# Optimization experiments

Measured on AMD Instinct MI355X. Metric: run time of the kernel, lower is better.

Reference implementation:

```python
import jax, jax.numpy as jnp
import numpy as np

EPS_STAB = 1e-9   # numerical_stabilizer default
BN_EPS = 1e-5     # flax BatchNorm default epsilon


def setup_inputs() -> dict:
    key = jax.random.key(0)
    ks = jax.random.split(key, 5)
    B, N, C = 2, 4096, 512
    s = 1.0 / np.sqrt(C)
    d = {"inputs": jax.random.normal(ks[0], (B, N, C), jnp.float32)}
    # 1x1 convs == pointwise linear maps [C_in, C_out] + bias
    for i, w in enumerate(["Wq", "Wk", "Wv", "Wo"]):
        d[w] = jax.random.normal(ks[1 + i], (C, C), jnp.float32) * s
    for b in ["bq", "bk", "bv", "bo"]:
        d[b] = jnp.zeros((C,), jnp.float32)
    # BatchNorm (inference: use_running_average=True since train=False)
    d["bn_scale"] = jnp.ones((C,), jnp.float32)
    d["bn_bias"] = jnp.zeros((C,), jnp.float32)
    d["bn_mean"] = jnp.zeros((C,), jnp.float32)
    d["bn_var"] = jnp.ones((C,), jnp.float32)
    return d


def reference(inputs, Wq, bq, Wk, bk, Wv, bv, Wo, bo,
              bn_scale, bn_bias, bn_mean, bn_var):
    # QKV via 1x1 conv == dense projection. [B, N, C]
    q = inputs @ Wq + bq
    k = inputs @ Wk + bk
    v = inputs @ Wv + bv
    # scores [B, M, N]; softmax over last axis (N)
    att = jax.nn.softmax(jnp.einsum('bmc,bnc->bmn', q, k), axis=-1)
    # non-standard renorm: divide by column sums (axis=1 == M axis)
    att = att / (EPS_STAB + jnp.sum(att, axis=1, keepdims=True))
    # faithful to einsum '...MN,...NC->...NC': sum attention over M, scale v
    out = v * jnp.sum(att, axis=1)[..., None]
    # output 1x1 conv
    out = out @ Wo + bo
    # BatchNorm with running stats (feature axis -1)
    out = (out - bn_mean) * jax.lax.rsqrt(bn_var + BN_EPS) * bn_scale + bn_bias
    return jax.nn.relu(out) + inputs
```

## Files before the change

### kernel.cpp

```cpp
#include <hip/hip_runtime.h>
#include <hip/hip_bf16.h>

typedef unsigned short u16;
typedef unsigned int u32;
typedef __attribute__((ext_vector_type(8))) short short8;
typedef __attribute__((ext_vector_type(4))) float f32x4;

__device__ __forceinline__ u16 f2bf(float f) {
    union { float f; unsigned u; } v; v.f = f;
    unsigned r = v.u + 0x7fffu + ((v.u >> 16) & 1u);
    return (u16)(r >> 16);
}

__device__ __forceinline__ float fexp2(float x) {
#if __has_builtin(__builtin_amdgcn_exp2f)
    return __builtin_amdgcn_exp2f(x);
#else
    return __expf(x * 0.6931471805599453f);
#endif
}

#if __has_builtin(__builtin_amdgcn_cvt_pk_fp8_f32) && \
    __has_builtin(__builtin_amdgcn_cvt_f32_fp8)
#define FP8_HW 1
#else
#define FP8_HW 0
#endif

#if !FP8_HW
__device__ __forceinline__ u32 sw_fp8(float x) {
    union { float f; u32 u; } v; v.f = x;
    int E = (int)(v.u >> 23) - 127;
    if (x < 0.001953125f) return 0;
    if (E < -6) return (u32)(x * 512.0f + 0.5f);
    u32 m = v.u & 0x7fffffu;
    u32 r = (m + 0x80000u) >> 20;
    u32 bits = ((u32)(E + 7) << 3) + r;
    return bits > 0x7eu ? 0x7eu : bits;
}
__device__ __forceinline__ float sw_fp8d(u32 b) {
    u32 e = (b >> 3) & 15u, m = b & 7u;
    if (e == 0) return (float)m * 0.001953125f;
    union { u32 u; float f; } v; v.u = ((e + 120u) << 23) | (m << 20);
    return v.f;
}
#endif

__device__ __forceinline__ u32 fp8x4_pack(float p0, float p1, float p2, float p3) {
#if FP8_HW
    u32 v = (u32)__builtin_amdgcn_cvt_pk_fp8_f32(p0, p1, 0, false);
    v = (u32)__builtin_amdgcn_cvt_pk_fp8_f32(p2, p3, (int)v, true);
    return v;
#else
    return sw_fp8(p0) | (sw_fp8(p1) << 8) | (sw_fp8(p2) << 16) | (sw_fp8(p3) << 24);
#endif
}

#if FP8_HW
#define FP8_DEC(v, s) __builtin_amdgcn_cvt_f32_fp8((int)(v), (s))
#else
#define FP8_DEC(v, s) sw_fp8d(((v) >> ((s) * 8)) & 0xffu)
#endif

__device__ __forceinline__ void async_cp16(const u16* g, u16* l) {
    __builtin_amdgcn_global_load_lds(
        (const __attribute__((address_space(1))) void*)g,
        (__attribute__((address_space(3))) void*)l, 16, 0, 0);
}


__device__ __forceinline__ void gemm512(const u16* __restrict__ A,
                                        const u16* __restrict__ B,
                                        u16* As, u16* Bs,
                                        f32x4 acc[4][4], int tid) {
    const int lane = tid & 63, w = tid >> 6;
    const int quad = lane >> 4, l15 = lane & 15;
    const int wm = tid >> 7, wn = (tid >> 6) & 1;
    const int Gw = lane ^ ((lane >> 3) & 7);
    const int srow = Gw >> 2;
    const int scol = (Gw & 3) * 8;
    const int arow0 = w * 32 + srow, arow1 = arow0 + 16;
    u16* la0 = As + (w * 2 + 0) * 512;
    u16* la1 = As + (w * 2 + 1) * 512;
    u16* lb0 = Bs + (w * 2 + 0) * 512;
    u16* lb1 = Bs + (w * 2 + 1) * 512;
    const int Pr8 = ((l15 * 4 + quad) ^ (l15 >> 1)) * 8;
    for (int k0 = 0; k0 < 512; k0 += 32) {
        __syncthreads();
        async_cp16(A + (size_t)arow0 * 512 + k0 + scol, la0);
        async_cp16(A + (size_t)arow1 * 512 + k0 + scol, la1);
        async_cp16(B + (size_t)arow0 * 512 + k0 + scol, lb0);
        async_cp16(B + (size_t)arow1 * 512 + k0 + scol, lb1);
        __syncthreads();
        short8 af[4], bfr[4];
#pragma unroll
        for (int i = 0; i < 4; i++)
            af[i] = *(const short8*)&As[(wm * 64 + i * 16) * 32 + Pr8];
#pragma unroll
        for (int j = 0; j < 4; j++)
            bfr[j] = *(const short8*)&Bs[(wn * 64 + j * 16) * 32 + Pr8];
#pragma unroll
        for (int i = 0; i < 4; i++)
#pragma unroll
            for (int j = 0; j < 4; j++)
                acc[i][j] = __builtin_amdgcn_mfma_f32_16x16x32_bf16(
                    af[i], bfr[j], acc[i][j], 0, 0, 0);
    }
}

__device__ __forceinline__ void gemm512_r64(const u16* __restrict__ A,
                                            const u16* __restrict__ B,
                                            u16* As, u16* Bs,
                                            f32x4 acc[2][4], int tid) {
    const int lane = tid & 63, w = tid >> 6;
    const int quad = lane >> 4, l15 = lane & 15;
    const int wm = tid >> 7, wn = (tid >> 6) & 1;
    const int Gw = lane ^ ((lane >> 3) & 7);
    const int srow = Gw >> 2;
    const int scol = (Gw & 3) * 8;
    const int arowA = w * 16 + srow;
    const int arowB0 = (w * 2 + 0) * 16 + srow;
    const int arowB1 = (w * 2 + 1) * 16 + srow;
    u16* la = As + w * 512;
    u16* lb0 = Bs + (w * 2 + 0) * 512;
    u16* lb1 = Bs + (w * 2 + 1) * 512;
    const int Pr8 = ((l15 * 4 + quad) ^ (l15 >> 1)) * 8;
    for (int k0 = 0; k0 < 512; k0 += 32) {
        __syncthreads();
        async_cp16(A + (size_t)arowA * 512 + k0 + scol, la);
        async_cp16(B + (size_t)arowB0 * 512 + k0 + scol, lb0);
        async_cp16(B + (size_t)arowB1 * 512 + k0 + scol, lb1);
        __syncthreads();
        short8 af[2], bfr[4];
#pragma unroll
        for (int i = 0; i < 2; i++)
            af[i] = *(const short8*)&As[(wm * 32 + i * 16) * 32 + Pr8];
#pragma unroll
        for (int j = 0; j < 4; j++)
            bfr[j] = *(const short8*)&Bs[(wn * 64 + j * 16) * 32 + Pr8];
#pragma unroll
        for (int i = 0; i < 2; i++)
#pragma unroll
            for (int j = 0; j < 4; j++)
                acc[i][j] = __builtin_amdgcn_mfma_f32_16x16x32_bf16(
                    af[i], bfr[j], acc[i][j], 0, 0, 0);
    }
}

__global__ void prep(const float* __restrict__ X, const float* __restrict__ W0,
                     const float* __restrict__ W1, const float* __restrict__ W2,
                     const float* __restrict__ W3, u16* __restrict__ Xb,
                     u16* __restrict__ T0, u16* __restrict__ T1,
                     u16* __restrict__ T2, u16* __restrict__ T3,
                     float* __restrict__ Sg) {
    __shared__ float tile[32][33];
    int id = blockIdx.x, tid = threadIdx.x;
    if (id == 5120) {
        float4 z = {0.f, 0.f, 0.f, 0.f};
#pragma unroll
        for (int t = 0; t < 8; t++) ((float4*)Sg)[tid + t * 256] = z;
        return;
    }
    if (id < 4096) {
        int idx = (id * 256 + tid) * 4;
        float4 v = *(const float4*)&X[idx];
        ushort4 o;
        o.x = f2bf(v.x); o.y = f2bf(v.y); o.z = f2bf(v.z); o.w = f2bf(v.w);
        *(ushort4*)&Xb[idx] = o;
        return;
    }
    int t = id - 4096;
    int z = t >> 8, rem = t & 255;
    int bo_ = (rem & 15) * 32, bi = (rem >> 4) * 32;
    const float* src; u16* dst;
    switch (z) {
        case 0: src = W0; dst = T0; break;
        case 1: src = W1; dst = T1; break;
        case 2: src = W2; dst = T2; break;
        default: src = W3; dst = T3; break;
    }
    int tx = tid & 31, ty = tid >> 5;
#pragma unroll
    for (int s = 0; s < 4; s++) {
        int i = bi + ty + s * 8;
        tile[ty + s * 8][tx] = src[i * 512 + bo_ + tx];
    }
    __syncthreads();
#pragma unroll
    for (int s = 0; s < 4; s++) {
        int o = bo_ + ty + s * 8;
        dst[o * 512 + bi + tx] = f2bf(tile[tx][ty + s * 8]);
    }
}

__global__ __launch_bounds__(256) void gemm_qkv(
    const u16* __restrict__ Xb, const u16* __restrict__ Wall,
    const float* __restrict__ bq, const float* __restrict__ bk,
    const float* __restrict__ bv, u16* __restrict__ Qall) {
    __shared__ __align__(16) u16 As[128 * 32];
    __shared__ __align__(16) u16 Bs[128 * 32];
    int tid = threadIdx.x;
    int m0 = blockIdx.x * 128, n0 = blockIdx.y * 128, z = blockIdx.z;
    const u16* Bt = Wall + (size_t)z * 262144 + (size_t)n0 * 512;
    const float* bias = (z == 0) ? bq : (z == 1) ? bk : bv;
    const float qs = (z == 0) ? 1.44269504088896340736f : 1.0f;
    u16* C = Qall + (size_t)z * 4194304;
    f32x4 acc[4][4];
#pragma unroll
    for (int i = 0; i < 4; i++)
#pragma unroll
        for (int j = 0; j < 4; j++) acc[i][j] = (f32x4){0.f, 0.f, 0.f, 0.f};
    gemm512(Xb + (size_t)m0 * 512, Bt, As, Bs, acc, tid);
    int lane = tid & 63, quad = lane >> 4, l15 = lane & 15;
    int wm = tid >> 7, wn = (tid >> 6) & 1;
#pragma unroll
    for (int j = 0; j < 4; j++) {
        int n = n0 + wn * 64 + j * 16 + l15;
        float bvv = bias[n];
#pragma unroll
        for (int i = 0; i < 4; i++)
#pragma unroll
            for (int rg = 0; rg < 4; rg++) {
                int m = m0 + wm * 64 + i * 16 + quad * 4 + rg;
                C[(size_t)m * 512 + n] = f2bf((acc[i][j][rg] + bvv) * qs);
            }
    }
}

__global__ __launch_bounds__(256) void attn_pass1p(
    const u16* __restrict__ Qb, const u16* __restrict__ Kb,
    float2* __restrict__ statsP, u32* __restrict__ Pbuf) {
    __shared__ __align__(16) u16 As[128 * 32];
    __shared__ __align__(16) u16 Bs[128 * 32];
    int tid = threadIdx.x;
    int mblk = blockIdx.x, nch = blockIdx.y, b = blockIdx.z;
    const u16* Q = Qb + ((size_t)(b * 4096 + mblk * 128)) * 512;
    int lane = tid & 63, quad = lane >> 4, l15 = lane & 15;
    int wm = tid >> 7, wn = (tid >> 6) & 1;
    for (int nt = 0; nt < 2; nt++) {
        const u16* K = Kb + ((size_t)(b * 4096 + nch * 256 + nt * 128)) * 512;
        f32x4 acc[4][4];
#pragma unroll
        for (int i = 0; i < 4; i++)
#pragma unroll
            for (int j = 0; j < 4; j++) acc[i][j] = (f32x4){0.f, 0.f, 0.f, 0.f};
        gemm512(Q, K, As, Bs, acc, tid);
        u32* Pt = Pbuf + (((size_t)(b * 32 + mblk) * 16 + nch) * 2 + nt) * 4096;
        int ch = nch * 4 + nt * 2 + wn;
#pragma unroll
        for (int i = 0; i < 4; i++)
#pragma unroll
            for (int rg = 0; rg < 4; rg++) {
                float v0 = acc[i][0][rg], v1 = acc[i][1][rg];
                float v2 = acc[i][2][rg], v3 = acc[i][3][rg];
                float Mt = fmaxf(fmaxf(v0, v1), fmaxf(v2, v3));
                Mt = fmaxf(Mt, __shfl_xor(Mt, 1));
                Mt = fmaxf(Mt, __shfl_xor(Mt, 2));
                Mt = fmaxf(Mt, __shfl_xor(Mt, 4));
                Mt = fmaxf(Mt, __shfl_xor(Mt, 8));
                float e8 = Mt - 8.0f;
                float p0 = fexp2(v0 - e8), p1 = fexp2(v1 - e8);
                float p2 = fexp2(v2 - e8), p3 = fexp2(v3 - e8);
                Pt[(i * 4 + rg) * 256 + tid] = fp8x4_pack(p0, p1, p2, p3);
                float L = p0 + p1 + p2 + p3;
                L += __shfl_xor(L, 1);
                L += __shfl_xor(L, 2);
                L += __shfl_xor(L, 4);
                L += __shfl_xor(L, 8);
                if (l15 == 0)
                    statsP[((size_t)(b * 64 + ch)) * 4096 + mblk * 128 +
                           wm * 64 + i * 16 + quad * 4 + rg] =
                        make_float2(Mt, L * 0.00390625f);
            }
    }
}

__global__ __launch_bounds__(256) void colsum_fused(
    const u32* __restrict__ Pbuf, const float2* __restrict__ statsP,
    float* __restrict__ Sg) {
    __shared__ float cbuf[512];
    int tid = threadIdx.x, lane = tid & 63;
    int wm = tid >> 7, wn = (tid >> 6) & 1, quad = lane >> 4;
    int nch = blockIdx.x, nt = blockIdx.y & 1, mgrp = blockIdx.y >> 1;
    int b = blockIdx.z;
    int ch = nch * 4 + nt * 2 + wn;
#pragma unroll
    for (int h = 0; h < 2; h++) {
        int row = mgrp * 512 + h * 256 + tid;
        const float2* sp = statsP + (size_t)b * 64 * 4096 + row;
        float M = -INFINITY;
#pragma unroll 4
        for (int c2 = 0; c2 < 64; c2++) M = fmaxf(M, sp[(size_t)c2 * 4096].x);
        float Z = 0.f;
#pragma unroll 4
        for (int c2 = 0; c2 < 64; c2++) {
            float2 p = sp[(size_t)c2 * 4096];
            Z += p.y * fexp2(p.x - M);
        }
        cbuf[h * 256 + tid] = M + __log2f(Z);
    }
    __syncthreads();
    const float2* Sp = statsP + ((size_t)(b * 64 + ch)) * 4096;
    float cp[4] = {0.f, 0.f, 0.f, 0.f};
    for (int mb = 0; mb < 4; mb++) {
        int mblk = mgrp * 4 + mb;
        const u32* Pt =
            Pbuf + (((size_t)(b * 32 + mblk) * 16 + nch) * 2 + nt) * 4096;
#pragma unroll
        for (int i = 0; i < 4; i++) {
            int r0 = mblk * 128 + wm * 64 + i * 16 + quad * 4;
            float4 s01 = *(const float4*)&Sp[r0];
            float4 s23 = *(const float4*)&Sp[r0 + 2];
            float4 cv = *(const float4*)&cbuf[r0 - mgrp * 512];
            float fv[4] = {fexp2(s01.x - 8.0f - cv.x),
                           fexp2(s01.z - 8.0f - cv.y),
                           fexp2(s23.x - 8.0f - cv.z),
                           fexp2(s23.z - 8.0f - cv.w)};
#pragma unroll
            for (int rg = 0; rg < 4; rg++) {
                u32 e = Pt[(i * 4 + rg) * 256 + tid];
                cp[0] += FP8_DEC(e, 0) * fv[rg];
                cp[1] += FP8_DEC(e, 1) * fv[rg];
                cp[2] += FP8_DEC(e, 2) * fv[rg];
                cp[3] += FP8_DEC(e, 3) * fv[rg];
            }
        }
    }
#pragma unroll
    for (int j = 0; j < 4; j++) {
        float s = cp[j];
        s += __shfl_xor(s, 16);
        s += __shfl_xor(s, 32);
        if (lane < 16)
            atomicAdd(&Sg[b * 4096 + nch * 256 + nt * 128 + wn * 64 + j * 16 + lane], s);
    }
}

__global__ __launch_bounds__(256) void legacy_pass1(
    const u16* __restrict__ Qb, const u16* __restrict__ Kb,
    float2* __restrict__ statsP) {
    __shared__ __align__(16) u16 As[128 * 32];
    __shared__ __align__(16) u16 Bs[128 * 32];
    int tid = threadIdx.x;
    int mblk = blockIdx.x, nch = blockIdx.y, b = blockIdx.z;
    const u16* Q = Qb + ((size_t)(b * 4096 + mblk * 128)) * 512;
    int lane = tid & 63, quad = lane >> 4, l15 = lane & 15;
    int wm = tid >> 7, wn = (tid >> 6) & 1;
    float runM[4][4], runL[4][4];
#pragma unroll
    for (int i = 0; i < 4; i++)
#pragma unroll
        for (int rg = 0; rg < 4; rg++) { runM[i][rg] = -INFINITY; runL[i][rg] = 0.f; }
    for (int nt = 0; nt < 2; nt++) {
        const u16* K = Kb + ((size_t)(b * 4096 + nch * 256 + nt * 128)) * 512;
        f32x4 acc[4][4];
#pragma unroll
        for (int i = 0; i < 4; i++)
#pragma unroll
            for (int j = 0; j < 4; j++) acc[i][j] = (f32x4){0.f, 0.f, 0.f, 0.f};
        gemm512(Q, K, As, Bs, acc, tid);
#pragma unroll
        for (int i = 0; i < 4; i++)
#pragma unroll
            for (int rg = 0; rg < 4; rg++) {
                float v0 = acc[i][0][rg], v1 = acc[i][1][rg];
                float v2 = acc[i][2][rg], v3 = acc[i][3][rg];
                float vm = fmaxf(fmaxf(v0, v1), fmaxf(v2, v3));
                float mo = runM[i][rg];
                if (vm > mo - 30.f) {
                    float nm = fmaxf(mo, vm);
                    runL[i][rg] = runL[i][rg] * fexp2(mo - nm) +
                                  fexp2(v0 - nm) + fexp2(v1 - nm) +
                                  fexp2(v2 - nm) + fexp2(v3 - nm);
                    runM[i][rg] = nm;
                }
            }
    }
#pragma unroll
    for (int i = 0; i < 4; i++)
#pragma unroll
        for (int rg = 0; rg < 4; rg++) {
            float M = runM[i][rg];
            float Mf = M;
#pragma unroll
            for (int d = 1; d < 16; d <<= 1) Mf = fmaxf(Mf, __shfl_xor(Mf, d));
            float L = runL[i][rg] * fexp2(M - Mf);
#pragma unroll
            for (int d = 1; d < 16; d <<= 1) L += __shfl_xor(L, d);
            if (l15 == 0)
                statsP[((size_t)(b * 32 + nch * 2 + wn)) * 4096 +
                       mblk * 128 + wm * 64 + i * 16 + quad * 4 + rg] =
                    make_float2(Mf, L);
        }
}

__global__ void legacy_reduce(const float2* __restrict__ statsP,
                              float* __restrict__ cstat, float* __restrict__ Sg) {
    int t = blockIdx.x * 256 + threadIdx.x;
    int b = t >> 12, m = t & 4095;
    const float2* sp = statsP + (size_t)b * 32 * 4096 + m;
    float M = -INFINITY;
#pragma unroll 4
    for (int ch = 0; ch < 32; ch++) M = fmaxf(M, sp[(size_t)ch * 4096].x);
    float L = 0.f;
#pragma unroll 4
    for (int ch = 0; ch < 32; ch++) {
        float2 p = sp[(size_t)ch * 4096];
        L += p.y * fexp2(p.x - M);
    }
    cstat[t] = M + __log2f(L);
    Sg[t] = 0.f;
}

__global__ __launch_bounds__(256) void legacy_pass2(
    const u16* __restrict__ Qb, const u16* __restrict__ Kb,
    const float* __restrict__ cstat, float* __restrict__ Sg) {
    __shared__ __align__(16) u16 As[128 * 32];
    __shared__ __align__(16) u16 Bs[128 * 32];
    int tid = threadIdx.x;
    int nblk = blockIdx.x, mch = blockIdx.y, b = blockIdx.z;
    const u16* K = Kb + ((size_t)(b * 4096 + nblk * 128)) * 512;
    int lane = tid & 63, quad = lane >> 4;
    int wm = tid >> 7, wn = (tid >> 6) & 1;
    float cp0 = 0.f, cp1 = 0.f, cp2 = 0.f, cp3 = 0.f;
    for (int mt = 0; mt < 2; mt++) {
        int m0 = mch * 256 + mt * 128;
        const u16* Q = Qb + ((size_t)(b * 4096 + m0)) * 512;
        f32x4 acc[4][4];
#pragma unroll
        for (int i = 0; i < 4; i++)
#pragma unroll
            for (int j = 0; j < 4; j++) acc[i][j] = (f32x4){0.f, 0.f, 0.f, 0.f};
        gemm512(Q, K, As, Bs, acc, tid);
        float4 c4[4];
#pragma unroll
        for (int i = 0; i < 4; i++)
            c4[i] = *(const float4*)&cstat[b * 4096 + m0 + wm * 64 + i * 16 + quad * 4];
#pragma unroll
        for (int i = 0; i < 4; i++) {
            float cc[4] = {c4[i].x, c4[i].y, c4[i].z, c4[i].w};
#pragma unroll
            for (int rg = 0; rg < 4; rg++) {
                float c = cc[rg];
                float v0 = acc[i][0][rg] - c, v1 = acc[i][1][rg] - c;
                float v2 = acc[i][2][rg] - c, v3 = acc[i][3][rg] - c;
                float vm = fmaxf(fmaxf(v0, v1), fmaxf(v2, v3));
                if (vm > -60.f) {
                    cp0 += fexp2(v0); cp1 += fexp2(v1);
                    cp2 += fexp2(v2); cp3 += fexp2(v3);
                }
            }
        }
    }
    float cps[4] = {cp0, cp1, cp2, cp3};
#pragma unroll
    for (int j = 0; j < 4; j++) {
        float s = cps[j];
        s += __shfl_xor(s, 16);
        s += __shfl_xor(s, 32);
        if (lane < 16)
            atomicAdd(&Sg[b * 4096 + nblk * 128 + wn * 64 + j * 16 + lane], s);
    }
}

__global__ __launch_bounds__(256) void gemm_final(
    const u16* __restrict__ A, const u16* __restrict__ Bt,
    const float* __restrict__ Sg, const float* __restrict__ bo,
    const float* __restrict__ g, const float* __restrict__ bb,
    const float* __restrict__ mean, const float* __restrict__ var,
    const float* __restrict__ X, float* __restrict__ out) {
    __shared__ __align__(16) u16 As[64 * 32];
    __shared__ __align__(16) u16 Bs[128 * 32];
    int tid = threadIdx.x;
    int m0 = blockIdx.x * 64, n0 = blockIdx.y * 128;
    f32x4 acc[2][4];
#pragma unroll
    for (int i = 0; i < 2; i++)
#pragma unroll
        for (int j = 0; j < 4; j++) acc[i][j] = (f32x4){0.f, 0.f, 0.f, 0.f};
    gemm512_r64(A + (size_t)m0 * 512, Bt + (size_t)n0 * 512, As, Bs, acc, tid);
    int lane = tid & 63, quad = lane >> 4, l15 = lane & 15;
    int wm = tid >> 7, wn = (tid >> 6) & 1;
    float sc[2][4];
#pragma unroll
    for (int i = 0; i < 2; i++) {
        float4 s = *(const float4*)&Sg[m0 + wm * 32 + i * 16 + quad * 4];
        float v[4] = {s.x, s.y, s.z, s.w};
#pragma unroll
        for (int rg = 0; rg < 4; rg++) sc[i][rg] = v[rg] / (1e-9f + v[rg]);
    }
#pragma unroll
    for (int j = 0; j < 4; j++) {
        int n = n0 + wn * 64 + j * 16 + l15;
        float aj = rsqrtf(var[n] + 1e-5f) * g[n];
        float cj = bb[n] - mean[n] * aj;
        float bj = bo[n];
#pragma unroll
        for (int i = 0; i < 2; i++)
#pragma unroll
            for (int rg = 0; rg < 4; rg++) {
                int m = m0 + wm * 32 + i * 16 + quad * 4 + rg;
                float x = acc[i][j][rg] * sc[i][rg] + bj;
                float y = x * aj + cj;
                out[(size_t)m * 512 + n] = fmaxf(y, 0.f) + X[(size_t)m * 512 + n];
            }
    }
}

extern "C" void kernel_launch(void* const* d_in, const int* in_sizes, int n_in,
                              void* d_out, int out_size, void* d_ws, size_t ws_size,
                              hipStream_t stream) {
    const float* X  = (const float*)d_in[0];
    const float* Wq = (const float*)d_in[1];
    const float* Wk = (const float*)d_in[2];
    const float* Wv = (const float*)d_in[3];
    const float* Wo = (const float*)d_in[4];
    const float* bq = (const float*)d_in[5];
    const float* bk = (const float*)d_in[6];
    const float* bv = (const float*)d_in[7];
    const float* bo = (const float*)d_in[8];
    const float* g    = (const float*)d_in[9];
    const float* bb   = (const float*)d_in[10];
    const float* mean = (const float*)d_in[11];
    const float* var  = (const float*)d_in[12];
    float* out = (float*)d_out;

    char* ws = (char*)d_ws;
    u16* Xb  = (u16*)(ws + 0);
    u16* Wqt = (u16*)(ws + 8388608);
    u16* Wot = (u16*)(ws + 9961472);
    u16* Qb  = (u16*)(ws + 10485760);
    u16* Kb  = (u16*)(ws + 18874368);
    u16* Vb  = (u16*)(ws + 27262976);
    float2* statsP = (float2*)(ws + 35651584);
    float* Sg      = (float*)(ws + 39845888);
    float* cstat   = (float*)(ws + 39878656);
    u32* Pbuf      = (u32*)(ws + 39911424);

    const size_t FULL_NEED = 39911424ull + 33554432ull;

    prep<<<5121, 256, 0, stream>>>(X, Wq, Wk, Wv, Wo, Xb, Wqt, Wqt + 262144,
                                   Wqt + 524288, Wot, Sg);
    gemm_qkv<<<dim3(64, 4, 3), 256, 0, stream>>>(Xb, Wqt, bq, bk, bv, Qb);

    if (ws_size >= FULL_NEED) {
        attn_pass1p<<<dim3(32, 16, 2), 256, 0, stream>>>(Qb, Kb, statsP, Pbuf);
        colsum_fused<<<dim3(16, 16, 2), 256, 0, stream>>>(Pbuf, statsP, Sg);
    } else {
        legacy_pass1<<<dim3(32, 16, 2), 256, 0, stream>>>(Qb, Kb, statsP);
        legacy_reduce<<<32, 256, 0, stream>>>(statsP, cstat, Sg);
        legacy_pass2<<<dim3(32, 16, 2), 256, 0, stream>>>(Qb, Kb, cstat, Sg);
    }
    gemm_final<<<dim3(128, 4), 256, 0, stream>>>(Vb, Wot, Sg, bo, g, bb, mean, var,
                                                 X, out);
}
```

Baseline: 232.5 us.

## Split row-stat reduction into its own kernel and skip negligible colsum tiles

Moves the per-row softmax normaliser (max and log-sum over 64 channel chunks) out of the colsum kernel into a separate small kernel. Before, each colsum block recomputed it for its rows, which was redundant across blocks. The colsum grid doubles so each block handles two m-blocks instead of four. Row groups whose scale factors are all below a tiny threshold now skip the FP8 loads and accumulation. The costs are an extra launch and a global round trip for cstat, and the skip drops contributions that are tiny but not zero.

```diff
diff --git a/kernel.cpp b/kernel.cpp
--- a/kernel.cpp
+++ b/kernel.cpp
@@ -275,35 +275,36 @@
     }
 }
 
-__global__ __launch_bounds__(256) void colsum_fused(
+__global__ void reduce_stats2(const float2* __restrict__ statsP,
+                              float* __restrict__ cstat) {
+    int t = blockIdx.x * 256 + threadIdx.x;
+    int b = t >> 12, m = t & 4095;
+    const float2* sp = statsP + (size_t)b * 64 * 4096 + m;
+    float M = -INFINITY;
+#pragma unroll 4
+    for (int ch = 0; ch < 64; ch++) M = fmaxf(M, sp[(size_t)ch * 4096].x);
+    float Z = 0.f;
+#pragma unroll 4
+    for (int ch = 0; ch < 64; ch++) {
+        float2 p = sp[(size_t)ch * 4096];
+        Z += p.y * fexp2(p.x - M);
+    }
+    cstat[t] = M + __log2f(Z);
+}
+
+__global__ __launch_bounds__(256) void colsum(
     const u32* __restrict__ Pbuf, const float2* __restrict__ statsP,
-    float* __restrict__ Sg) {
-    __shared__ float cbuf[512];
+    const float* __restrict__ cstat, float* __restrict__ Sg) {
     int tid = threadIdx.x, lane = tid & 63;
     int wm = tid >> 7, wn = (tid >> 6) & 1, quad = lane >> 4;
     int nch = blockIdx.x, nt = blockIdx.y & 1, mgrp = blockIdx.y >> 1;
     int b = blockIdx.z;
     int ch = nch * 4 + nt * 2 + wn;
-#pragma unroll
-    for (int h = 0; h < 2; h++) {
-        int row = mgrp * 512 + h * 256 + tid;
-        const float2* sp = statsP + (size_t)b * 64 * 4096 + row;
-        float M = -INFINITY;
-#pragma unroll 4
-        for (int c2 = 0; c2 < 64; c2++) M = fmaxf(M, sp[(size_t)c2 * 4096].x);
-        float Z = 0.f;
-#pragma unroll 4
-        for (int c2 = 0; c2 < 64; c2++) {
-            float2 p = sp[(size_t)c2 * 4096];
-            Z += p.y * fexp2(p.x - M);
-        }
-        cbuf[h * 256 + tid] = M + __log2f(Z);
-    }
-    __syncthreads();
     const float2* Sp = statsP + ((size_t)(b * 64 + ch)) * 4096;
+    const float* Cp = cstat + (size_t)b * 4096;
     float cp[4] = {0.f, 0.f, 0.f, 0.f};
-    for (int mb = 0; mb < 4; mb++) {
-        int mblk = mgrp * 4 + mb;
+    for (int mb = 0; mb < 2; mb++) {
+        int mblk = mgrp * 2 + mb;
         const u32* Pt =
             Pbuf + (((size_t)(b * 32 + mblk) * 16 + nch) * 2 + nt) * 4096;
 #pragma unroll
@@ -311,18 +312,21 @@
             int r0 = mblk * 128 + wm * 64 + i * 16 + quad * 4;
             float4 s01 = *(const float4*)&Sp[r0];
             float4 s23 = *(const float4*)&Sp[r0 + 2];
-            float4 cv = *(const float4*)&cbuf[r0 - mgrp * 512];
+            float4 cv = *(const float4*)&Cp[r0];
             float fv[4] = {fexp2(s01.x - 8.0f - cv.x),
                            fexp2(s01.z - 8.0f - cv.y),
                            fexp2(s23.x - 8.0f - cv.z),
                            fexp2(s23.z - 8.0f - cv.w)};
-#pragma unroll
-            for (int rg = 0; rg < 4; rg++) {
-                u32 e = Pt[(i * 4 + rg) * 256 + tid];
-                cp[0] += FP8_DEC(e, 0) * fv[rg];
-                cp[1] += FP8_DEC(e, 1) * fv[rg];
-                cp[2] += FP8_DEC(e, 2) * fv[rg];
-                cp[3] += FP8_DEC(e, 3) * fv[rg];
+            float fm = fmaxf(fmaxf(fv[0], fv[1]), fmaxf(fv[2], fv[3]));
+            if (fm > 3.469446951953614e-18f) {
+#pragma unroll
+                for (int rg = 0; rg < 4; rg++) {
+                    u32 e = Pt[(i * 4 + rg) * 256 + tid];
+                    cp[0] += FP8_DEC(e, 0) * fv[rg];
+                    cp[1] += FP8_DEC(e, 1) * fv[rg];
+                    cp[2] += FP8_DEC(e, 2) * fv[rg];
+                    cp[3] += FP8_DEC(e, 3) * fv[rg];
+                }
             }
         }
     }
@@ -545,7 +549,8 @@
 
     if (ws_size >= FULL_NEED) {
         attn_pass1p<<<dim3(32, 16, 2), 256, 0, stream>>>(Qb, Kb, statsP, Pbuf);
-        colsum_fused<<<dim3(16, 16, 2), 256, 0, stream>>>(Pbuf, statsP, Sg);
+        reduce_stats2<<<32, 256, 0, stream>>>(statsP, cstat);
+        colsum<<<dim3(16, 32, 2), 256, 0, stream>>>(Pbuf, statsP, cstat, Sg);
     } else {
         legacy_pass1<<<dim3(32, 16, 2), 256, 0, stream>>>(Qb, Kb, statsP);
         legacy_reduce<<<32, 256, 0, stream>>>(statsP, cstat, Sg);
```

After: 215.7 us. 1.08x faster.

## Fuse attention pass and column-sum via grid-wide barrier, keep P in registers

Applied to the files above, without the earlier changes.

Merges the score/exp pass and the column-sum pass into one kernel. Each block now covers four key tiles and keeps the fp8 probabilities in registers, so the 32 MB Pbuf round trip through global memory disappears. A global atomic-counter spin barrier waits for all 512 blocks to publish their row stats before the per-row logsumexp is computed. Row groups whose scale factor is negligible skip the decode-and-accumulate. The barrier only works if all 512 blocks are resident at once, which launch_bounds(256,2) is meant to ensure; it deadlocks otherwise, and the extra registers for P may cause spilling.

```diff
diff --git a/kernel.cpp b/kernel.cpp
--- a/kernel.cpp
+++ b/kernel.cpp
@@ -67,7 +67,6 @@
         (const __attribute__((address_space(1))) void*)g,
         (__attribute__((address_space(3))) void*)l, 16, 0, 0);
 }
-
 
 __device__ __forceinline__ void gemm512(const u16* __restrict__ A,
                                         const u16* __restrict__ B,
@@ -152,10 +151,11 @@
                      const float* __restrict__ W3, u16* __restrict__ Xb,
                      u16* __restrict__ T0, u16* __restrict__ T1,
                      u16* __restrict__ T2, u16* __restrict__ T3,
-                     float* __restrict__ Sg) {
+                     float* __restrict__ Sg, u32* __restrict__ counter) {
     __shared__ float tile[32][33];
     int id = blockIdx.x, tid = threadIdx.x;
     if (id == 5120) {
+        if (tid == 0) *counter = 0;
         float4 z = {0.f, 0.f, 0.f, 0.f};
 #pragma unroll
         for (int t = 0; t < 8; t++) ((float4*)Sg)[tid + t * 256] = z;
@@ -227,17 +227,23 @@
     }
 }
 
-__global__ __launch_bounds__(256) void attn_pass1p(
+__global__ __launch_bounds__(256, 2) void attn_fused2(
     const u16* __restrict__ Qb, const u16* __restrict__ Kb,
-    float2* __restrict__ statsP, u32* __restrict__ Pbuf) {
+    float2* __restrict__ statsP, float* __restrict__ Sg,
+    u32* __restrict__ counter) {
     __shared__ __align__(16) u16 As[128 * 32];
     __shared__ __align__(16) u16 Bs[128 * 32];
+    __shared__ float mtbuf[4][2][128];
+    __shared__ float cbuf[128];
     int tid = threadIdx.x;
-    int mblk = blockIdx.x, nch = blockIdx.y, b = blockIdx.z;
+    int mblk = blockIdx.x, nch2 = blockIdx.y, b = blockIdx.z;
     const u16* Q = Qb + ((size_t)(b * 4096 + mblk * 128)) * 512;
     int lane = tid & 63, quad = lane >> 4, l15 = lane & 15;
     int wm = tid >> 7, wn = (tid >> 6) & 1;
-    for (int nt = 0; nt < 2; nt++) {
+    u32 P[4][16];
+#pragma unroll
+    for (int t = 0; t < 4; t++) {
+        int nch = nch2 * 2 + (t >> 1), nt = t & 1;
         const u16* K = Kb + ((size_t)(b * 4096 + nch * 256 + nt * 128)) * 512;
         f32x4 acc[4][4];
 #pragma unroll
@@ -245,7 +251,6 @@
 #pragma unroll
             for (int j = 0; j < 4; j++) acc[i][j] = (f32x4){0.f, 0.f, 0.f, 0.f};
         gemm512(Q, K, As, Bs, acc, tid);
-        u32* Pt = Pbuf + (((size_t)(b * 32 + mblk) * 16 + nch) * 2 + nt) * 4096;
         int ch = nch * 4 + nt * 2 + wn;
 #pragma unroll
         for (int i = 0; i < 4; i++)
@@ -261,33 +266,36 @@
                 float e8 = Mt - 8.0f;
                 float p0 = fexp2(v0 - e8), p1 = fexp2(v1 - e8);
                 float p2 = fexp2(v2 - e8), p3 = fexp2(v3 - e8);
-                Pt[(i * 4 + rg) * 256 + tid] = fp8x4_pack(p0, p1, p2, p3);
+                P[t][i * 4 + rg] = fp8x4_pack(p0, p1, p2, p3);
                 float L = p0 + p1 + p2 + p3;
                 L += __shfl_xor(L, 1);
                 L += __shfl_xor(L, 2);
                 L += __shfl_xor(L, 4);
                 L += __shfl_xor(L, 8);
-                if (l15 == 0)
-                    statsP[((size_t)(b * 64 + ch)) * 4096 + mblk * 128 +
-                           wm * 64 + i * 16 + quad * 4 + rg] =
+                if (l15 == 0) {
+                    int r = wm * 64 + i * 16 + quad * 4 + rg;
+                    statsP[((size_t)(b * 64 + ch)) * 4096 + mblk * 128 + r] =
                         make_float2(Mt, L * 0.00390625f);
+                    mtbuf[t][wn][r] = Mt;
+                }
             }
     }
-}
-
-__global__ __launch_bounds__(256) void colsum_fused(
-    const u32* __restrict__ Pbuf, const float2* __restrict__ statsP,
-    float* __restrict__ Sg) {
-    __shared__ float cbuf[512];
-    int tid = threadIdx.x, lane = tid & 63;
-    int wm = tid >> 7, wn = (tid >> 6) & 1, quad = lane >> 4;
-    int nch = blockIdx.x, nt = blockIdx.y & 1, mgrp = blockIdx.y >> 1;
-    int b = blockIdx.z;
-    int ch = nch * 4 + nt * 2 + wn;
-#pragma unroll
-    for (int h = 0; h < 2; h++) {
-        int row = mgrp * 512 + h * 256 + tid;
-        const float2* sp = statsP + (size_t)b * 64 * 4096 + row;
+    __syncthreads();
+    __threadfence();
+    if (tid == 0) {
+        __hip_atomic_fetch_add(counter, 1u, __ATOMIC_ACQ_REL,
+                               __HIP_MEMORY_SCOPE_AGENT);
+        int it = 0;
+        while (__hip_atomic_load(counter, __ATOMIC_ACQUIRE,
+                                 __HIP_MEMORY_SCOPE_AGENT) < 512u &&
+               it < (1 << 24)) {
+            __builtin_amdgcn_s_sleep(2);
+            ++it;
+        }
+    }
+    __syncthreads();
+    if (tid < 128) {
+        const float2* sp = statsP + (size_t)b * 64 * 4096 + mblk * 128 + tid;
         float M = -INFINITY;
 #pragma unroll 4
         for (int c2 = 0; c2 < 64; c2++) M = fmaxf(M, sp[(size_t)c2 * 4096].x);
@@ -297,42 +305,45 @@
             float2 p = sp[(size_t)c2 * 4096];
             Z += p.y * fexp2(p.x - M);
         }
-        cbuf[h * 256 + tid] = M + __log2f(Z);
+        cbuf[tid] = M + __log2f(Z);
     }
     __syncthreads();
-    const float2* Sp = statsP + ((size_t)(b * 64 + ch)) * 4096;
-    float cp[4] = {0.f, 0.f, 0.f, 0.f};
-    for (int mb = 0; mb < 4; mb++) {
-        int mblk = mgrp * 4 + mb;
-        const u32* Pt =
-            Pbuf + (((size_t)(b * 32 + mblk) * 16 + nch) * 2 + nt) * 4096;
+#pragma unroll
+    for (int t = 0; t < 4; t++) {
+        float cp[4] = {0.f, 0.f, 0.f, 0.f};
+        bool any = false;
 #pragma unroll
         for (int i = 0; i < 4; i++) {
-            int r0 = mblk * 128 + wm * 64 + i * 16 + quad * 4;
-            float4 s01 = *(const float4*)&Sp[r0];
-            float4 s23 = *(const float4*)&Sp[r0 + 2];
-            float4 cv = *(const float4*)&cbuf[r0 - mgrp * 512];
-            float fv[4] = {fexp2(s01.x - 8.0f - cv.x),
-                           fexp2(s01.z - 8.0f - cv.y),
-                           fexp2(s23.x - 8.0f - cv.z),
-                           fexp2(s23.z - 8.0f - cv.w)};
-#pragma unroll
-            for (int rg = 0; rg < 4; rg++) {
-                u32 e = Pt[(i * 4 + rg) * 256 + tid];
-                cp[0] += FP8_DEC(e, 0) * fv[rg];
-                cp[1] += FP8_DEC(e, 1) * fv[rg];
-                cp[2] += FP8_DEC(e, 2) * fv[rg];
-                cp[3] += FP8_DEC(e, 3) * fv[rg];
+            int rb = wm * 64 + i * 16 + quad * 4;
+            float F0 = fexp2(mtbuf[t][wn][rb + 0] - 8.0f - cbuf[rb + 0]);
+            float F1 = fexp2(mtbuf[t][wn][rb + 1] - 8.0f - cbuf[rb + 1]);
+            float F2 = fexp2(mtbuf[t][wn][rb + 2] - 8.0f - cbuf[rb + 2]);
+            float F3 = fexp2(mtbuf[t][wn][rb + 3] - 8.0f - cbuf[rb + 3]);
+            float fm = fmaxf(fmaxf(F0, F1), fmaxf(F2, F3));
+            if (fm > 3.469446951953614e-18f) {
+                any = true;
+                float Fv[4] = {F0, F1, F2, F3};
+#pragma unroll
+                for (int rg = 0; rg < 4; rg++) {
+                    u32 e = P[t][i * 4 + rg];
+                    cp[0] += FP8_DEC(e, 0) * Fv[rg];
+                    cp[1] += FP8_DEC(e, 1) * Fv[rg];
+                    cp[2] += FP8_DEC(e, 2) * Fv[rg];
+                    cp[3] += FP8_DEC(e, 3) * Fv[rg];
+                }
             }
         }
-    }
-#pragma unroll
-    for (int j = 0; j < 4; j++) {
-        float s = cp[j];
-        s += __shfl_xor(s, 16);
-        s += __shfl_xor(s, 32);
-        if (lane < 16)
-            atomicAdd(&Sg[b * 4096 + nch * 256 + nt * 128 + wn * 64 + j * 16 + lane], s);
+        (void)any;
+#pragma unroll
+        for (int j = 0; j < 4; j++) {
+            float s = cp[j];
+            s += __shfl_xor(s, 16);
+            s += __shfl_xor(s, 32);
+            if (lane < 16)
+                atomicAdd(&Sg[b * 4096 + nch2 * 512 + t * 128 + wn * 64 +
+                              j * 16 + lane],
+                          s);
+        }
     }
 }
 
@@ -535,17 +546,17 @@
     float2* statsP = (float2*)(ws + 35651584);
     float* Sg      = (float*)(ws + 39845888);
     float* cstat   = (float*)(ws + 39878656);
-    u32* Pbuf      = (u32*)(ws + 39911424);
-
-    const size_t FULL_NEED = 39911424ull + 33554432ull;
+    u32* counter   = (u32*)(ws + 39911424);
+
+    const size_t FULL_NEED = 39911424ull + 64ull;
 
     prep<<<5121, 256, 0, stream>>>(X, Wq, Wk, Wv, Wo, Xb, Wqt, Wqt + 262144,
-                                   Wqt + 524288, Wot, Sg);
+                                   Wqt + 524288, Wot, Sg, counter);
     gemm_qkv<<<dim3(64, 4, 3), 256, 0, stream>>>(Xb, Wqt, bq, bk, bv, Qb);
 
     if (ws_size >= FULL_NEED) {
-        attn_pass1p<<<dim3(32, 16, 2), 256, 0, stream>>>(Qb, Kb, statsP, Pbuf);
-        colsum_fused<<<dim3(16, 16, 2), 256, 0, stream>>>(Pbuf, statsP, Sg);
+        attn_fused2<<<dim3(32, 8, 2), 256, 0, stream>>>(Qb, Kb, statsP, Sg,
+                                                        counter);
     } else {
         legacy_pass1<<<dim3(32, 16, 2), 256, 0, stream>>>(Qb, Kb, statsP);
         legacy_reduce<<<32, 256, 0, stream>>>(statsP, cstat, Sg);
```

After: 268.1 us. 1.15x slower.
